# Kernel tuning notes

Measured on AMD Instinct MI355X. Metric: run time of the kernel, lower is better.

The kernel has to match this reference:

```python
import jax, jax.numpy as jnp
import numpy as np

N, E, D_IN, HID, H, L = 20000, 320000, 64, 128, 4, 3
D_HEAD = HID  # PyG TransformerConv: out_channels is the per-head dim
LN_EPS = 1e-5


def setup_inputs() -> dict:
    key = jax.random.key(0)
    ks = jax.random.split(key, 12)
    x = jax.random.normal(ks[0], (N, D_IN), dtype=jnp.float32)
    edge_index = jax.random.randint(ks[1], (2, E), 0, N, dtype=jnp.int64)
    s_in = 1.0 / np.sqrt(D_IN)
    s_h = 1.0 / np.sqrt(HID)
    Win = jax.random.normal(ks[2], (D_IN, HID), dtype=jnp.float32) * s_in
    bin_ = jnp.zeros((HID,), dtype=jnp.float32)
    Wq = jax.random.normal(ks[3], (L, HID, H * D_HEAD), dtype=jnp.float32) * s_h
    Wk = jax.random.normal(ks[4], (L, HID, H * D_HEAD), dtype=jnp.float32) * s_h
    Wv = jax.random.normal(ks[5], (L, HID, H * D_HEAD), dtype=jnp.float32) * s_h
    bq = jnp.zeros((L, H * D_HEAD), dtype=jnp.float32)
    bk = jnp.zeros((L, H * D_HEAD), dtype=jnp.float32)
    bv = jnp.zeros((L, H * D_HEAD), dtype=jnp.float32)
    Wskip = jax.random.normal(ks[6], (L, HID, HID), dtype=jnp.float32) * s_h
    bskip = jnp.zeros((L, HID), dtype=jnp.float32)
    ln_gamma = jnp.ones((L, HID), dtype=jnp.float32)
    ln_beta = jnp.zeros((L, HID), dtype=jnp.float32)
    return dict(x=x, edge_index=edge_index, Win=Win, bin_=bin_, Wq=Wq, bq=bq,
                Wk=Wk, bk=bk, Wv=Wv, bv=bv, Wskip=Wskip, bskip=bskip,
                ln_gamma=ln_gamma, ln_beta=ln_beta)


def _segment_softmax(logits, seg, num_segments):
    # logits: [E, H], seg: [E] destination node ids
    m = jax.ops.segment_max(logits, seg, num_segments=num_segments)  # [N, H]
    ex = jnp.exp(logits - m[seg])
    s = jax.ops.segment_sum(ex, seg, num_segments=num_segments)  # [N, H]
    return ex / (s[seg] + 1e-16)


def _layer_norm(x, gamma, beta):
    mu = jnp.mean(x, axis=-1, keepdims=True)
    var = jnp.mean(jnp.square(x - mu), axis=-1, keepdims=True)
    return (x - mu) * jax.lax.rsqrt(var + LN_EPS) * gamma + beta


def _transformer_conv(h, src, dst, Wq, bq, Wk, bk, Wv, bv, Wskip, bskip):
    q = (h @ Wq + bq).reshape(N, H, D_HEAD)
    k = (h @ Wk + bk).reshape(N, H, D_HEAD)
    v = (h @ Wv + bv).reshape(N, H, D_HEAD)
    scale = 1.0 / np.sqrt(D_HEAD)
    logits = jnp.einsum('ehd,ehd->eh', q[dst], k[src]) * scale  # [E, H]
    alpha = _segment_softmax(logits, dst, N)  # [E, H]
    msg = alpha[:, :, None] * v[src]  # [E, H, D_HEAD]
    out = jax.ops.segment_sum(msg, dst, num_segments=N)  # [N, H, D_HEAD]
    out = out.mean(axis=1)  # concat=False -> mean over heads
    return out + h @ Wskip + bskip  # root_weight skip (lin_skip)


def reference(x, edge_index, Win, bin_, Wq, bq, Wk, bk, Wv, bv, Wskip, bskip, ln_gamma, ln_beta):
    src = edge_index[0]
    dst = edge_index[1]
    h = x @ Win + bin_
    for l in range(L):
        h_new = _transformer_conv(h, src, dst, Wq[l], bq[l], Wk[l], bk[l],
                                  Wv[l], bv[l], Wskip[l], bskip[l])
        h = _layer_norm(h + h_new, ln_gamma[l], ln_beta[l])
    return h
```

## Files before the change

kernel.cpp:

```cpp
#include <hip/hip_runtime.h>
#include <hip/hip_bf16.h>
#include <math.h>

#define NN 20000
#define EE 320000
#define DIN 64
#define HIDC 128
#define NCOLS 1664
#define NL 3
#define LG2SCALE 0.12751659601518297f

typedef __attribute__((ext_vector_type(8))) short bf16x8;
typedef __attribute__((ext_vector_type(8))) unsigned short u16x8;
typedef __attribute__((ext_vector_type(4))) float f32x4;

__device__ __forceinline__ float bf2f(unsigned short u) {
  union { unsigned i; float f; } v; v.i = ((unsigned)u) << 16; return v.f;
}
__device__ __forceinline__ unsigned short f2bf(float f) {
  __hip_bfloat16 b = __float2bfloat16(f);
  return *(unsigned short*)&b;
}

__device__ __forceinline__ unsigned char f2fp8(float f) {
#if __has_builtin(__builtin_amdgcn_cvt_pk_fp8_f32)
  return (unsigned char)(__builtin_amdgcn_cvt_pk_fp8_f32(f, f, 0, 0) & 0xFF);
#else
  unsigned b = __float_as_uint(f);
  unsigned s = (b >> 24) & 0x80u;
  float a = fabsf(f);
  if (a < 0.015625f) return (unsigned char)s;
  unsigned mag = __float_as_uint(fminf(a, 448.f));
  mag += 0x7FFFFu + ((mag >> 20) & 1u);
  unsigned code = (mag >> 20) - (120u << 3);
  if (code > 0x7Eu) code = 0x7Eu;
  return (unsigned char)(s | code);
#endif
}

__device__ __forceinline__ float fp82f(unsigned b) {
  unsigned x = ((b & 0x80u) << 24) | ((b & 0x7fu) << 20);
  return __uint_as_float(x) * 0x1p+120f;
}

__device__ __forceinline__ void dec8(uint2 u, float* f) {
#if __has_builtin(__builtin_amdgcn_cvt_pk_f32_fp8)
  {
    auto p0 = __builtin_amdgcn_cvt_pk_f32_fp8(u.x, 0);
    auto p1 = __builtin_amdgcn_cvt_pk_f32_fp8(u.x, 1);
    auto p2 = __builtin_amdgcn_cvt_pk_f32_fp8(u.y, 0);
    auto p3 = __builtin_amdgcn_cvt_pk_f32_fp8(u.y, 1);
    f[0] = p0[0]; f[1] = p0[1]; f[2] = p1[0]; f[3] = p1[1];
    f[4] = p2[0]; f[5] = p2[1]; f[6] = p3[0]; f[7] = p3[1];
  }
#else
#pragma unroll
  for (int i = 0; i < 4; i++) f[i] = fp82f((u.x >> (8 * i)) & 0xFFu);
#pragma unroll
  for (int i = 0; i < 4; i++) f[4 + i] = fp82f((u.y >> (8 * i)) & 0xFFu);
#endif
}

__global__ void build_wcatT_all(const float* __restrict__ Wq, const float* __restrict__ Wk,
                                const float* __restrict__ Wv, const float* __restrict__ Wsk,
                                unsigned short* __restrict__ wT) {
  int idx = blockIdx.x * 256 + threadIdx.x;
  if (idx >= NL * NCOLS * HIDC) return;
  int l = idx / (NCOLS * HIDC);
  int rem = idx - l * (NCOLS * HIDC);
  int n = rem >> 7, k = rem & 127;
  float v;
  if (n < 512)       v = Wq[(size_t)l * HIDC * 512 + (size_t)k * 512 + n];
  else if (n < 1024) v = Wk[(size_t)l * HIDC * 512 + (size_t)k * 512 + (n - 512)];
  else if (n < 1536) v = Wv[(size_t)l * HIDC * 512 + (size_t)k * 512 + (n - 1024)];
  else               v = Wsk[(size_t)l * HIDC * HIDC + (size_t)k * 128 + (n - 1536)];
  wT[idx] = f2bf(v);
}

__global__ void build_bcat_all(const float* __restrict__ bq, const float* __restrict__ bk,
                               const float* __restrict__ bv, const float* __restrict__ bsk,
                               float* __restrict__ bcat) {
  int idx = blockIdx.x * 256 + threadIdx.x;
  if (idx >= NL * NCOLS) return;
  int l = idx / NCOLS, m = idx - l * NCOLS;
  float v;
  if (m < 512)       v = bq[l * 512 + m];
  else if (m < 1024) v = bk[l * 512 + (m - 512)];
  else if (m < 1536) v = bv[l * 512 + (m - 1024)];
  else               v = bsk[l * 128 + (m - 1536)];
  bcat[idx] = v;
}

__global__ void build_winT(const float* __restrict__ Win, unsigned short* __restrict__ winT) {
  int idx = blockIdx.x * 256 + threadIdx.x;
  if (idx >= HIDC * DIN) return;
  int c = idx >> 6, k = idx & 63;
  winT[idx] = f2bf(Win[(size_t)k * HIDC + c]);
}

__global__ void conv_x(const float* __restrict__ x, unsigned short* __restrict__ xb) {
  int i = blockIdx.x * 256 + threadIdx.x;
  if (i * 4 >= NN * DIN) return;
  float4 v = *(const float4*)(x + (size_t)i * 4);
  ushort4 o = make_ushort4(f2bf(v.x), f2bf(v.y), f2bf(v.z), f2bf(v.w));
  *(ushort4*)(xb + (size_t)i * 4) = o;
}

__global__ void deg_hist(const int* __restrict__ ei, int* __restrict__ deg) {
  int e = blockIdx.x * 256 + threadIdx.x;
  if (e >= EE) return;
  atomicAdd(&deg[ei[EE + e]], 1);
}

__global__ __launch_bounds__(1024) void scan_deg(const int* __restrict__ deg,
                                                 int* __restrict__ rowstart) {
  __shared__ int part[1024];
  int t = threadIdx.x;
  int base = t * 20;
  int local[20];
  int s = 0;
#pragma unroll
  for (int i = 0; i < 20; i++) {
    int idx = base + i;
    int d = (idx < NN) ? deg[idx] : 0;
    local[i] = d;
    s += d;
  }
  part[t] = s;
  __syncthreads();
  for (int d = 1; d < 1024; d <<= 1) {
    int v = (t >= d) ? part[t - d] : 0;
    __syncthreads();
    part[t] += v;
    __syncthreads();
  }
  int run = part[t] - s;
#pragma unroll
  for (int i = 0; i < 20; i++) {
    int idx = base + i;
    if (idx < NN) rowstart[idx] = run;
    run += local[i];
  }
  if (t == 1023) rowstart[NN] = part[1023];
}

__global__ void csr_scatter(const int* __restrict__ ei, const int* __restrict__ rowstart,
                            int* __restrict__ cur, int* __restrict__ csrc) {
  int e = blockIdx.x * 256 + threadIdx.x;
  if (e >= EE) return;
  int src = ei[e], dst = ei[EE + e];
  int pos = atomicAdd(&cur[dst], 1);
  csrc[rowstart[dst] + pos] = src << 10;
}

__device__ __forceinline__ void gl_lds16(const void* g, void* l) {
  __builtin_amdgcn_global_load_lds((const unsigned int*)g, (unsigned int*)l, 16, 0, 0);
}

template <int K>
__device__ __forceinline__ void stage_tile(const unsigned short* gbase,
                                           unsigned char* lbase, int tid) {
  constexpr int CH = K / 8;
  constexpr int ISS = (128 * CH) / 256;
  int wave = tid >> 6;
#pragma unroll
  for (int p = 0; p < ISS; p++) {
    int slot = p * 256 + tid;
    int row = slot / CH, ch = slot % CH;
    const unsigned short* src = gbase + (size_t)row * K + ((ch ^ (row & 7)) * 8);
    unsigned char* ldst = lbase + (size_t)(p * 256 + wave * 64) * 16;
    gl_lds16(src, ldst);
  }
}

template <int K>
__device__ __forceinline__ bf16x8 read_frag(const unsigned char* lbase, int row, int kk, int lk) {
  int ch = (kk * 4 + lk) ^ (row & 7);
  return *(const bf16x8*)(lbase + (size_t)row * (K * 2) + ch * 16);
}

__global__ __launch_bounds__(256) void mfma_gemm_in(
    const unsigned short* __restrict__ A, const unsigned short* __restrict__ BT,
    const float* __restrict__ bias, unsigned short* __restrict__ outb,
    float* __restrict__ outf) {
  __shared__ __align__(16) unsigned char LDS[34816];
  const int tid = threadIdx.x;
  const int lane = tid & 63, wave = tid >> 6;
  const int lm = lane & 15, lk = lane >> 4;
  const int wm = wave >> 1, wn = wave & 1;
  const int row0 = blockIdx.x * 128;
  unsigned char* aL = LDS;
  unsigned char* bL = LDS + 128 * 64 * 2;

  stage_tile<64>(A + (size_t)row0 * 64, aL, tid);
  stage_tile<64>(BT, bL, tid);
  __syncthreads();

  f32x4 acc[4][4] = {};
  bf16x8 af[4][2];
#pragma unroll
  for (int mf = 0; mf < 4; mf++)
#pragma unroll
    for (int kk = 0; kk < 2; kk++)
      af[mf][kk] = read_frag<64>(aL, wm * 64 + mf * 16 + lm, kk, lk);
#pragma unroll
  for (int nf = 0; nf < 4; nf++) {
    bf16x8 bf[2];
#pragma unroll
    for (int kk = 0; kk < 2; kk++)
      bf[kk] = read_frag<64>(bL, wn * 64 + nf * 16 + lm, kk, lk);
#pragma unroll
    for (int mf = 0; mf < 4; mf++)
#pragma unroll
      for (int kk = 0; kk < 2; kk++)
        acc[mf][nf] = __builtin_amdgcn_mfma_f32_16x16x32_bf16(af[mf][kk], bf[kk],
                                                              acc[mf][nf], 0, 0, 0);
  }
  __syncthreads();

  unsigned short* bb = (unsigned short*)LDS;
#pragma unroll
  for (int nf = 0; nf < 4; nf++) {
    int c = wn * 64 + nf * 16 + lm;
    float bv = bias[c];
#pragma unroll
    for (int mf = 0; mf < 4; mf++)
#pragma unroll
      for (int i = 0; i < 4; i++) {
        int row = wm * 64 + mf * 16 + lk * 4 + i;
        float o = acc[mf][nf][i] + bv;
        bb[row * 136 + c] = f2bf(o);
        int r = row0 + row;
        if (r < NN) outf[(size_t)r * HIDC + c] = o;
      }
  }
  __syncthreads();
#pragma unroll
  for (int p = 0; p < 8; p++) {
    int idx = p * 256 + tid;
    int row = idx >> 4, c = idx & 15;
    int gr = row0 + row;
    if (gr < NN) {
      uint4 v = *(const uint4*)(bb + row * 136 + c * 8);
      *(uint4*)(outb + (size_t)gr * HIDC + c * 8) = v;
    }
  }
}

__global__ __launch_bounds__(256, 5) void gemm64(
    const unsigned short* __restrict__ A, const unsigned short* __restrict__ BT,
    const float* __restrict__ bias, unsigned short* __restrict__ qb,
    unsigned char* __restrict__ kv8, float* __restrict__ skipb,
    int nbx, int nwg) {
  __shared__ __align__(16) unsigned char LDS[32768];
  const int tid = threadIdx.x;
  int orig = blockIdx.x;
  int qq = nwg >> 3, rr8 = nwg & 7;
  int xcd = orig & 7, slot = orig >> 3;
  int wg = (xcd < rr8 ? xcd * (qq + 1) : rr8 * (qq + 1) + (xcd - rr8) * qq) + slot;
  const int bx = wg % nbx, by = wg / nbx;

  const int lane = tid & 63, wave = tid >> 6;
  const int lm = lane & 15, lk = lane >> 4;
  const int wm = wave >> 1, wn = wave & 1;
  const int row0 = by * 64, col0 = bx * 64;
  const int kvbase = (bx - 8) * 32;
  unsigned char* aL = LDS;
  unsigned char* bL = LDS + 16384;

  {
    const unsigned short* gA = A + (size_t)row0 * 128;
#pragma unroll
    for (int p = 0; p < 4; p++) {
      int sl = p * 256 + tid;
      int row = sl >> 4, ch = sl & 15;
      gl_lds16(gA + (size_t)row * 128 + ((ch ^ (row & 7)) * 8),
               aL + (size_t)(p * 256 + wave * 64) * 16);
    }
    if (bx >= 8 && bx < 24) {
#pragma unroll
      for (int p = 0; p < 4; p++) {
        int sl = p * 256 + tid;
        int row = sl >> 4, ch = sl & 15;
        int grow = (row < 32) ? (512 + kvbase + row) : (1024 + kvbase + row - 32);
        gl_lds16(BT + (size_t)grow * 128 + ((ch ^ (row & 7)) * 8),
                 bL + (size_t)(p * 256 + wave * 64) * 16);
      }
    } else {
      const unsigned short* gB = BT + (size_t)col0 * 128;
#pragma unroll
      for (int p = 0; p < 4; p++) {
        int sl = p * 256 + tid;
        int row = sl >> 4, ch = sl & 15;
        gl_lds16(gB + (size_t)row * 128 + ((ch ^ (row & 7)) * 8),
                 bL + (size_t)(p * 256 + wave * 64) * 16);
      }
    }
  }
  __syncthreads();

  f32x4 acc[2][2] = {};
  bf16x8 af[2][4], bf[2][4];
#pragma unroll
  for (int mf = 0; mf < 2; mf++)
#pragma unroll
    for (int kk = 0; kk < 4; kk++)
      af[mf][kk] = read_frag<128>(aL, wm * 32 + mf * 16 + lm, kk, lk);
#pragma unroll
  for (int nf = 0; nf < 2; nf++)
#pragma unroll
    for (int kk = 0; kk < 4; kk++)
      bf[nf][kk] = read_frag<128>(bL, wn * 32 + nf * 16 + lm, kk, lk);
#pragma unroll
  for (int nf = 0; nf < 2; nf++)
#pragma unroll
    for (int mf = 0; mf < 2; mf++)
#pragma unroll
      for (int kk = 0; kk < 4; kk++)
        acc[mf][nf] = __builtin_amdgcn_mfma_f32_16x16x32_bf16(af[mf][kk], bf[nf][kk],
                                                              acc[mf][nf], 0, 0, 0);
  __syncthreads();

  if (bx >= 24) {
    const int cbase = col0 - 1536;
#pragma unroll
    for (int nf = 0; nf < 2; nf++) {
      int c = wn * 32 + nf * 16 + lm;
      float bv = bias[col0 + c];
#pragma unroll
      for (int mf = 0; mf < 2; mf++)
#pragma unroll
        for (int i = 0; i < 4; i++) {
          int r = row0 + wm * 32 + mf * 16 + lk * 4 + i;
          if (r < NN) skipb[(size_t)r * HIDC + cbase + c] = acc[mf][nf][i] + bv;
        }
    }
  } else if (bx >= 8) {
    unsigned char* bb8 = LDS;
#pragma unroll
    for (int nf = 0; nf < 2; nf++) {
      int c = wn * 32 + nf * 16 + lm;
      int jj = c & 31;
      float bv = bias[(c < 32) ? (512 + kvbase + jj) : (1024 + kvbase + jj)];
      int lc = ((jj >> 3) << 4) + ((c < 32) ? 0 : 8) + (jj & 7);
#pragma unroll
      for (int mf = 0; mf < 2; mf++)
#pragma unroll
        for (int i = 0; i < 4; i++) {
          int row = wm * 32 + mf * 16 + lk * 4 + i;
          bb8[row * 80 + lc] = f2fp8(acc[mf][nf][i] + bv);
        }
    }
    __syncthreads();
    {
      int row = tid >> 2, cw = tid & 3;
      int gr = row0 + row;
      if (gr < NN) {
        uint4 v = *(const uint4*)(bb8 + row * 80 + cw * 16);
        *(uint4*)(kv8 + (size_t)gr * 1024 + 2 * kvbase + cw * 16) = v;
      }
    }
  } else {
    unsigned short* bb = (unsigned short*)LDS;
#pragma unroll
    for (int nf = 0; nf < 2; nf++) {
      int c = wn * 32 + nf * 16 + lm;
      float bv = bias[col0 + c];
#pragma unroll
      for (int mf = 0; mf < 2; mf++)
#pragma unroll
        for (int i = 0; i < 4; i++) {
          int row = wm * 32 + mf * 16 + lk * 4 + i;
          bb[row * 80 + c] = f2bf(acc[mf][nf][i] + bv);
        }
    }
    __syncthreads();
#pragma unroll
    for (int p = 0; p < 2; p++) {
      int idx = p * 256 + tid;
      int row = idx >> 3, cw = idx & 7;
      int gr = row0 + row;
      if (gr < NN) {
        uint4 v = *(const uint4*)(bb + row * 80 + cw * 8);
        *(uint4*)(qb + (size_t)gr * 512 + col0 + cw * 8) = v;
      }
    }
  }
}

__global__ __launch_bounds__(256) void node_fused(
    const unsigned short* __restrict__ qb, const unsigned char* __restrict__ kv8,
    const float* __restrict__ skipb,
    const float* __restrict__ h, const int* __restrict__ rowstart,
    const int* __restrict__ csrc,
    const float* __restrict__ gamma, const float* __restrict__ beta,
    float* __restrict__ outp, unsigned short* __restrict__ hb_out) {
  int n = blockIdx.x * 4 + (threadIdx.x >> 6);
  if (n >= NN) return;
  int lane = threadIdx.x & 63;
  int hh = lane >> 4, t = lane & 15;
  int j0 = rowstart[n], j1 = rowstart[n + 1];

  u16x8 q8 = *(const u16x8*)(qb + (size_t)n * 512 + hh * 128 + t * 8);
  float qf[8];
#pragma unroll
  for (int i = 0; i < 8; i++) qf[i] = bf2f(q8[i]);

  const unsigned char* kvp = kv8 + hh * 256 + t * 16;

  float m = -INFINITY, s = 0.f;
  float acc[8] = {0.f, 0.f, 0.f, 0.f, 0.f, 0.f, 0.f, 0.f};

  int j = j0;
  for (; j + 3 < j1; j += 4) {
    int s4[4];
#pragma unroll
    for (int e = 0; e < 4; e++) s4[e] = csrc[j + e];
    uint4 kv4[4];
#pragma unroll
    for (int e = 0; e < 4; e++) kv4[e] = *(const uint4*)(kvp + (size_t)s4[e]);
    float lg4[4];
#pragma unroll
    for (int e = 0; e < 4; e++) {
      float kf[8];
      dec8(make_uint2(kv4[e].x, kv4[e].y), kf);
      float p = 0.f;
#pragma unroll
      for (int i = 0; i < 8; i++) p += qf[i] * kf[i];
      p += __shfl_xor(p, 1);
      p += __shfl_xor(p, 2);
      p += __shfl_xor(p, 4);
      p += __shfl_xor(p, 8);
      lg4[e] = p * LG2SCALE;
    }
    float mx = fmaxf(fmaxf(lg4[0], lg4[1]), fmaxf(lg4[2], lg4[3]));
    if (mx > m) {
      float rr = exp2f(m - mx);
      s *= rr;
#pragma unroll
      for (int i = 0; i < 8; i++) acc[i] *= rr;
      m = mx;
    }
#pragma unroll
    for (int e = 0; e < 4; e++) {
      float w = exp2f(lg4[e] - m);
      s += w;
      float vf[8];
      dec8(make_uint2(kv4[e].z, kv4[e].w), vf);
#pragma unroll
      for (int i = 0; i < 8; i++) acc[i] += w * vf[i];
    }
  }
  for (; j < j1; ++j) {
    uint4 kv = *(const uint4*)(kvp + (size_t)csrc[j]);
    float kfA[8], vfA[8];
    dec8(make_uint2(kv.x, kv.y), kfA);
    dec8(make_uint2(kv.z, kv.w), vfA);
    float pA = 0.f;
#pragma unroll
    for (int i = 0; i < 8; i++) pA += qf[i] * kfA[i];
    pA += __shfl_xor(pA, 1);
    pA += __shfl_xor(pA, 2);
    pA += __shfl_xor(pA, 4);
    pA += __shfl_xor(pA, 8);
    float lgA = pA * LG2SCALE;
    if (lgA > m) {
      float rr = exp2f(m - lgA);
      s *= rr;
#pragma unroll
      for (int i = 0; i < 8; i++) acc[i] *= rr;
      m = lgA;
    }
    float wA = exp2f(lgA - m);
    s += wA;
#pragma unroll
    for (int i = 0; i < 8; i++) acc[i] += wA * vfA[i];
  }

  float rsel = 0.25f / (s + 1e-16f);
#pragma unroll
  for (int i = 0; i < 8; i++) {
    float a = acc[i] * rsel;
    a += __shfl_xor(a, 16);
    a += __shfl_xor(a, 32);
    acc[i] = a;
  }

  size_t hbase = (size_t)n * HIDC;
  float u[8];
  {
    float4 h0 = *(const float4*)(h + hbase + t * 8);
    float4 h1 = *(const float4*)(h + hbase + t * 8 + 4);
    float4 k0 = *(const float4*)(skipb + hbase + t * 8);
    float4 k1 = *(const float4*)(skipb + hbase + t * 8 + 4);
    u[0] = h0.x + acc[0] + k0.x; u[1] = h0.y + acc[1] + k0.y;
    u[2] = h0.z + acc[2] + k0.z; u[3] = h0.w + acc[3] + k0.w;
    u[4] = h1.x + acc[4] + k1.x; u[5] = h1.y + acc[5] + k1.y;
    u[6] = h1.z + acc[6] + k1.z; u[7] = h1.w + acc[7] + k1.w;
  }
  float su = 0.f;
#pragma unroll
  for (int i = 0; i < 8; i++) su += u[i];
#pragma unroll
  for (int d = 1; d < 16; d <<= 1) su += __shfl_xor(su, d);
  float mu = su * (1.f / 128.f);
  float vs = 0.f;
#pragma unroll
  for (int i = 0; i < 8; i++) { u[i] -= mu; vs += u[i] * u[i]; }
#pragma unroll
  for (int d = 1; d < 16; d <<= 1) vs += __shfl_xor(vs, d);
  float inv = rsqrtf(vs * (1.f / 128.f) + 1e-5f);
  if (hh == 0) {
    float4 g0 = *(const float4*)(gamma + t * 8);
    float4 g1 = *(const float4*)(gamma + t * 8 + 4);
    float4 b0 = *(const float4*)(beta + t * 8);
    float4 b1 = *(const float4*)(beta + t * 8 + 4);
    float o[8];
    o[0] = u[0] * inv * g0.x + b0.x; o[1] = u[1] * inv * g0.y + b0.y;
    o[2] = u[2] * inv * g0.z + b0.z; o[3] = u[3] * inv * g0.w + b0.w;
    o[4] = u[4] * inv * g1.x + b1.x; o[5] = u[5] * inv * g1.y + b1.y;
    o[6] = u[6] * inv * g1.z + b1.z; o[7] = u[7] * inv * g1.w + b1.w;
    *(float4*)(outp + hbase + t * 8)     = make_float4(o[0], o[1], o[2], o[3]);
    *(float4*)(outp + hbase + t * 8 + 4) = make_float4(o[4], o[5], o[6], o[7]);
    ushort4 c0 = make_ushort4(f2bf(o[0]), f2bf(o[1]), f2bf(o[2]), f2bf(o[3]));
    ushort4 c1 = make_ushort4(f2bf(o[4]), f2bf(o[5]), f2bf(o[6]), f2bf(o[7]));
    *(ushort4*)(hb_out + hbase + t * 8)     = c0;
    *(ushort4*)(hb_out + hbase + t * 8 + 4) = c1;
  }
}

#define OFF_H      ((size_t)0)
#define OFF_SKIP   ((size_t)2560000)
#define OFF_QB     ((size_t)5120000)
#define OFF_KV8    ((size_t)10240000)
#define OFF_HB     ((size_t)15360000)
#define OFF_XB     ((size_t)16640000)
#define OFF_WT     ((size_t)17280000)
#define OFF_WINT   ((size_t)17599488)
#define OFF_BCAT   ((size_t)17603584)
#define OFF_CSRC   ((size_t)17608576)
#define OFF_ROW    ((size_t)17928576)
#define OFF_DEG    ((size_t)17948580)
#define OFF_CUR    ((size_t)17968580)

extern "C" void kernel_launch(void* const* d_in, const int* in_sizes, int n_in,
                              void* d_out, int out_size, void* d_ws, size_t ws_size,
                              hipStream_t stream) {
  const float* x    = (const float*)d_in[0];
  const int*   ei   = (const int*)d_in[1];
  const float* Win  = (const float*)d_in[2];
  const float* bin_ = (const float*)d_in[3];
  const float* Wq   = (const float*)d_in[4];
  const float* bq   = (const float*)d_in[5];
  const float* Wk   = (const float*)d_in[6];
  const float* bk   = (const float*)d_in[7];
  const float* Wv   = (const float*)d_in[8];
  const float* bv   = (const float*)d_in[9];
  const float* Wsk  = (const float*)d_in[10];
  const float* bsk  = (const float*)d_in[11];
  const float* lng  = (const float*)d_in[12];
  const float* lnb  = (const float*)d_in[13];
  float* out = (float*)d_out;
  float* ws = (float*)d_ws;

  float* h     = ws + OFF_H;
  float* skipb = ws + OFF_SKIP;
  unsigned short* qb   = (unsigned short*)(ws + OFF_QB);
  unsigned char*  kv8  = (unsigned char*)(ws + OFF_KV8);
  unsigned short* hb   = (unsigned short*)(ws + OFF_HB);
  unsigned short* xb   = (unsigned short*)(ws + OFF_XB);
  unsigned short* wT   = (unsigned short*)(ws + OFF_WT);
  unsigned short* winT = (unsigned short*)(ws + OFF_WINT);
  float* bcat  = ws + OFF_BCAT;
  int* csrc     = (int*)(ws + OFF_CSRC);
  int* rowstart = (int*)(ws + OFF_ROW);
  int* deg      = (int*)(ws + OFF_DEG);
  int* cur      = (int*)(ws + OFF_CUR);

  hipMemsetAsync(deg, 0, NN * sizeof(int), stream);
  hipMemsetAsync(cur, 0, NN * sizeof(int), stream);
  deg_hist<<<(EE + 255) / 256, 256, 0, stream>>>(ei, deg);
  scan_deg<<<1, 1024, 0, stream>>>(deg, rowstart);
  csr_scatter<<<(EE + 255) / 256, 256, 0, stream>>>(ei, rowstart, cur, csrc);

  conv_x<<<(NN * DIN / 4 + 255) / 256, 256, 0, stream>>>(x, xb);
  build_winT<<<(HIDC * DIN + 255) / 256, 256, 0, stream>>>(Win, winT);
  build_wcatT_all<<<(NL * NCOLS * HIDC + 255) / 256, 256, 0, stream>>>(
      Wq, Wk, Wv, Wsk, wT);
  build_bcat_all<<<(NL * NCOLS + 255) / 256, 256, 0, stream>>>(bq, bk, bv, bsk, bcat);

  mfma_gemm_in<<<(NN + 127) / 128, 256, 0, stream>>>(xb, winT, bin_, hb, h);

  const int nbx = NCOLS / 64;
  const int nby = (NN + 63) / 64;
  const int nwg = nbx * nby;

  for (int l = 0; l < NL; ++l) {
    gemm64<<<nwg, 256, 0, stream>>>(hb, wT + (size_t)l * NCOLS * HIDC,
                                    bcat + (size_t)l * NCOLS, qb, kv8, skipb,
                                    nbx, nwg);

    float* dst = (l == NL - 1) ? out : h;
    node_fused<<<(NN + 3) / 4, 256, 0, stream>>>(
        qb, kv8, skipb, h, rowstart, csrc,
        lng + (size_t)l * 128, lnb + (size_t)l * 128, dst, hb);
  }
  (void)in_sizes; (void)n_in; (void)out_size; (void)ws_size;
}
```

Before: 312.7 us.

## Make GEMM blocks loop over column tiles reusing A fragments; fold residual into skip

```diff
diff --git a/kernel.cpp b/kernel.cpp
--- a/kernel.cpp
+++ b/kernel.cpp
@@ -247,26 +247,27 @@
   }
 }
 
-__global__ __launch_bounds__(256, 5) void gemm64(
+__global__ __launch_bounds__(256, 3) void gemm64p(
     const unsigned short* __restrict__ A, const unsigned short* __restrict__ BT,
-    const float* __restrict__ bias, unsigned short* __restrict__ qb,
-    unsigned char* __restrict__ kv8, float* __restrict__ skipb,
-    int nbx, int nwg) {
-  __shared__ __align__(16) unsigned char LDS[32768];
+    const float* __restrict__ bias, const float* __restrict__ hin,
+    unsigned short* __restrict__ qb, unsigned char* __restrict__ kv8,
+    float* __restrict__ skipb, int nwg) {
+  __shared__ __align__(16) unsigned char LDS[43008];
+  unsigned char* aL = LDS;
+  unsigned char* bL = LDS + 16384;
+  unsigned char* bnc = LDS + 32768;
   const int tid = threadIdx.x;
+
   int orig = blockIdx.x;
   int qq = nwg >> 3, rr8 = nwg & 7;
   int xcd = orig & 7, slot = orig >> 3;
   int wg = (xcd < rr8 ? xcd * (qq + 1) : rr8 * (qq + 1) + (xcd - rr8) * qq) + slot;
-  const int bx = wg % nbx, by = wg / nbx;
+  const int by = wg >> 1, half = wg & 1;
 
   const int lane = tid & 63, wave = tid >> 6;
   const int lm = lane & 15, lk = lane >> 4;
   const int wm = wave >> 1, wn = wave & 1;
-  const int row0 = by * 64, col0 = bx * 64;
-  const int kvbase = (bx - 8) * 32;
-  unsigned char* aL = LDS;
-  unsigned char* bL = LDS + 16384;
+  const int row0 = by * 64;
 
   {
     const unsigned short* gA = A + (size_t)row0 * 128;
@@ -277,6 +278,16 @@
       gl_lds16(gA + (size_t)row * 128 + ((ch ^ (row & 7)) * 8),
                aL + (size_t)(p * 256 + wave * 64) * 16);
     }
+  }
+
+  bf16x8 af[2][4];
+  bool afLoaded = false;
+
+  for (int it = 0; it < 13; ++it) {
+    const int bx = half * 13 + it;
+    const int col0 = bx * 64;
+    const int kvbase = (bx - 8) * 32;
+
     if (bx >= 8 && bx < 24) {
 #pragma unroll
       for (int p = 0; p < 4; p++) {
@@ -296,93 +307,100 @@
                  bL + (size_t)(p * 256 + wave * 64) * 16);
       }
     }
-  }
-  __syncthreads();
-
-  f32x4 acc[2][2] = {};
-  bf16x8 af[2][4], bf[2][4];
-#pragma unroll
-  for (int mf = 0; mf < 2; mf++)
-#pragma unroll
-    for (int kk = 0; kk < 4; kk++)
-      af[mf][kk] = read_frag<128>(aL, wm * 32 + mf * 16 + lm, kk, lk);
-#pragma unroll
-  for (int nf = 0; nf < 2; nf++)
-#pragma unroll
-    for (int kk = 0; kk < 4; kk++)
-      bf[nf][kk] = read_frag<128>(bL, wn * 32 + nf * 16 + lm, kk, lk);
-#pragma unroll
-  for (int nf = 0; nf < 2; nf++)
-#pragma unroll
-    for (int mf = 0; mf < 2; mf++)
-#pragma unroll
-      for (int kk = 0; kk < 4; kk++)
-        acc[mf][nf] = __builtin_amdgcn_mfma_f32_16x16x32_bf16(af[mf][kk], bf[nf][kk],
-                                                              acc[mf][nf], 0, 0, 0);
-  __syncthreads();
-
-  if (bx >= 24) {
-    const int cbase = col0 - 1536;
-#pragma unroll
-    for (int nf = 0; nf < 2; nf++) {
-      int c = wn * 32 + nf * 16 + lm;
-      float bv = bias[col0 + c];
+    __syncthreads();
+
+    if (!afLoaded) {
+      afLoaded = true;
 #pragma unroll
       for (int mf = 0; mf < 2; mf++)
 #pragma unroll
-        for (int i = 0; i < 4; i++) {
-          int r = row0 + wm * 32 + mf * 16 + lk * 4 + i;
-          if (r < NN) skipb[(size_t)r * HIDC + cbase + c] = acc[mf][nf][i] + bv;
+        for (int kk = 0; kk < 4; kk++)
+          af[mf][kk] = read_frag<128>(aL, wm * 32 + mf * 16 + lm, kk, lk);
+    }
+
+    f32x4 acc[2][2] = {};
+    {
+      bf16x8 bf[2][4];
+#pragma unroll
+      for (int nf = 0; nf < 2; nf++)
+#pragma unroll
+        for (int kk = 0; kk < 4; kk++)
+          bf[nf][kk] = read_frag<128>(bL, wn * 32 + nf * 16 + lm, kk, lk);
+#pragma unroll
+      for (int nf = 0; nf < 2; nf++)
+#pragma unroll
+        for (int mf = 0; mf < 2; mf++)
+#pragma unroll
+          for (int kk = 0; kk < 4; kk++)
+            acc[mf][nf] = __builtin_amdgcn_mfma_f32_16x16x32_bf16(af[mf][kk], bf[nf][kk],
+                                                                  acc[mf][nf], 0, 0, 0);
+    }
+
+    if (bx >= 24) {
+      const int cbase = col0 - 1536;
+#pragma unroll
+      for (int nf = 0; nf < 2; nf++) {
+        int c = wn * 32 + nf * 16 + lm;
+        float bv = bias[col0 + c];
+#pragma unroll
+        for (int mf = 0; mf < 2; mf++)
+#pragma unroll
+          for (int i = 0; i < 4; i++) {
+            int r = row0 + wm * 32 + mf * 16 + lk * 4 + i;
+            if (r < NN)
+              skipb[(size_t)r * HIDC + cbase + c] =
+                  acc[mf][nf][i] + bv + hin[(size_t)r * HIDC + cbase + c];
+          }
+      }
+      __syncthreads();
+    } else if (bx >= 8) {
+#pragma unroll
+      for (int nf = 0; nf < 2; nf++) {
+        int c = wn * 32 + nf * 16 + lm;
+        int jj = c & 31;
+        float bv = bias[(c < 32) ? (512 + kvbase + jj) : (1024 + kvbase + jj)];
+        int lc = ((jj >> 3) << 4) + ((c < 32) ? 0 : 8) + (jj & 7);
+#pragma unroll
+        for (int mf = 0; mf < 2; mf++)
+#pragma unroll
+          for (int i = 0; i < 4; i++) {
+            int row = wm * 32 + mf * 16 + lk * 4 + i;
+            bnc[row * 80 + lc] = f2fp8(acc[mf][nf][i] + bv);
+          }
+      }
+      __syncthreads();
+      {
+        int row = tid >> 2, cw = tid & 3;
+        int gr = row0 + row;
+        if (gr < NN) {
+          uint4 v = *(const uint4*)(bnc + row * 80 + cw * 16);
+          *(uint4*)(kv8 + (size_t)gr * 1024 + 2 * kvbase + cw * 16) = v;
         }
-    }
-  } else if (bx >= 8) {
-    unsigned char* bb8 = LDS;
-#pragma unroll
-    for (int nf = 0; nf < 2; nf++) {
-      int c = wn * 32 + nf * 16 + lm;
-      int jj = c & 31;
-      float bv = bias[(c < 32) ? (512 + kvbase + jj) : (1024 + kvbase + jj)];
-      int lc = ((jj >> 3) << 4) + ((c < 32) ? 0 : 8) + (jj & 7);
-#pragma unroll
-      for (int mf = 0; mf < 2; mf++)
-#pragma unroll
-        for (int i = 0; i < 4; i++) {
-          int row = wm * 32 + mf * 16 + lk * 4 + i;
-          bb8[row * 80 + lc] = f2fp8(acc[mf][nf][i] + bv);
+      }
+    } else {
+      unsigned short* bb = (unsigned short*)bnc;
+#pragma unroll
+      for (int nf = 0; nf < 2; nf++) {
+        int c = wn * 32 + nf * 16 + lm;
+        float bv = bias[col0 + c];
+#pragma unroll
+        for (int mf = 0; mf < 2; mf++)
+#pragma unroll
+          for (int i = 0; i < 4; i++) {
+            int row = wm * 32 + mf * 16 + lk * 4 + i;
+            bb[row * 80 + c] = f2bf(acc[mf][nf][i] + bv);
+          }
+      }
+      __syncthreads();
+#pragma unroll
+      for (int p = 0; p < 2; p++) {
+        int idx = p * 256 + tid;
+        int row = idx >> 3, cw = idx & 7;
+        int gr = row0 + row;
+        if (gr < NN) {
+          uint4 v = *(const uint4*)(bb + row * 80 + cw * 8);
+          *(uint4*)(qb + (size_t)gr * 512 + col0 + cw * 8) = v;
         }
-    }
-    __syncthreads();
-    {
-      int row = tid >> 2, cw = tid & 3;
-      int gr = row0 + row;
-      if (gr < NN) {
-        uint4 v = *(const uint4*)(bb8 + row * 80 + cw * 16);
-        *(uint4*)(kv8 + (size_t)gr * 1024 + 2 * kvbase + cw * 16) = v;
-      }
-    }
-  } else {
-    unsigned short* bb = (unsigned short*)LDS;
-#pragma unroll
-    for (int nf = 0; nf < 2; nf++) {
-      int c = wn * 32 + nf * 16 + lm;
-      float bv = bias[col0 + c];
-#pragma unroll
-      for (int mf = 0; mf < 2; mf++)
-#pragma unroll
-        for (int i = 0; i < 4; i++) {
-          int row = wm * 32 + mf * 16 + lk * 4 + i;
-          bb[row * 80 + c] = f2bf(acc[mf][nf][i] + bv);
-        }
-    }
-    __syncthreads();
-#pragma unroll
-    for (int p = 0; p < 2; p++) {
-      int idx = p * 256 + tid;
-      int row = idx >> 3, cw = idx & 7;
-      int gr = row0 + row;
-      if (gr < NN) {
-        uint4 v = *(const uint4*)(bb + row * 80 + cw * 8);
-        *(uint4*)(qb + (size_t)gr * 512 + col0 + cw * 8) = v;
       }
     }
   }
@@ -391,8 +409,7 @@
 __global__ __launch_bounds__(256) void node_fused(
     const unsigned short* __restrict__ qb, const unsigned char* __restrict__ kv8,
     const float* __restrict__ skipb,
-    const float* __restrict__ h, const int* __restrict__ rowstart,
-    const int* __restrict__ csrc,
+    const int* __restrict__ rowstart, const int* __restrict__ csrc,
     const float* __restrict__ gamma, const float* __restrict__ beta,
     float* __restrict__ outp, unsigned short* __restrict__ hb_out) {
   int n = blockIdx.x * 4 + (threadIdx.x >> 6);
@@ -489,14 +506,12 @@
   size_t hbase = (size_t)n * HIDC;
   float u[8];
   {
-    float4 h0 = *(const float4*)(h + hbase + t * 8);
-    float4 h1 = *(const float4*)(h + hbase + t * 8 + 4);
     float4 k0 = *(const float4*)(skipb + hbase + t * 8);
     float4 k1 = *(const float4*)(skipb + hbase + t * 8 + 4);
-    u[0] = h0.x + acc[0] + k0.x; u[1] = h0.y + acc[1] + k0.y;
-    u[2] = h0.z + acc[2] + k0.z; u[3] = h0.w + acc[3] + k0.w;
-    u[4] = h1.x + acc[4] + k1.x; u[5] = h1.y + acc[5] + k1.y;
-    u[6] = h1.z + acc[6] + k1.z; u[7] = h1.w + acc[7] + k1.w;
+    u[0] = acc[0] + k0.x; u[1] = acc[1] + k0.y;
+    u[2] = acc[2] + k0.z; u[3] = acc[3] + k0.w;
+    u[4] = acc[4] + k1.x; u[5] = acc[5] + k1.y;
+    u[6] = acc[6] + k1.z; u[7] = acc[7] + k1.w;
   }
   float su = 0.f;
 #pragma unroll
@@ -591,18 +606,17 @@
 
   mfma_gemm_in<<<(NN + 127) / 128, 256, 0, stream>>>(xb, winT, bin_, hb, h);
 
-  const int nbx = NCOLS / 64;
   const int nby = (NN + 63) / 64;
-  const int nwg = nbx * nby;
+  const int nwg = nby * 2;
 
   for (int l = 0; l < NL; ++l) {
-    gemm64<<<nwg, 256, 0, stream>>>(hb, wT + (size_t)l * NCOLS * HIDC,
-                                    bcat + (size_t)l * NCOLS, qb, kv8, skipb,
-                                    nbx, nwg);
+    gemm64p<<<nwg, 256, 0, stream>>>(hb, wT + (size_t)l * NCOLS * HIDC,
+                                     bcat + (size_t)l * NCOLS, h, qb, kv8, skipb,
+                                     nwg);
 
     float* dst = (l == NL - 1) ? out : h;
     node_fused<<<(NN + 3) / 4, 256, 0, stream>>>(
-        qb, kv8, skipb, h, rowstart, csrc,
+        qb, kv8, skipb, rowstart, csrc,
         lng + (size_t)l * 128, lnb + (size_t)l * 128, dst, hb);
   }
   (void)in_sizes; (void)n_in; (void)out_size; (void)ws_size;
```

Measured after the change: 318.3 us. Within noise of the previous version (+1.8%).
